# Kernel optimization log

Hardware: AMD Instinct MI355X
Metric: run time of the kernel (lower is better)

## Reference

```python
import jax, jax.numpy as jnp
import numpy as np

B, D, N = 2, 256, 8192   # batch, in_channels, sequence length
CI = 128                 # inter_channels
BN_EPS = 1e-5


def conv1x1(w, b, x):
    # w: (Cout, Cin), b: (Cout,), x: (B, Cin, N) -> (B, Cout, N)
    return jnp.einsum('oc,bcn->bon', w, x) + b[None, :, None]


def maxpool2(x):
    # MaxPool1d(kernel_size=2): (B, C, N) -> (B, C, N//2)
    b, c, n = x.shape
    return x.reshape(b, c, n // 2, 2).max(axis=-1)


def setup_inputs() -> dict:
    key = jax.random.key(0)
    ks = jax.random.split(key, 11)
    s_in = 1.0 / np.sqrt(D)
    s_ci = 1.0 / np.sqrt(CI)
    return {
        'f': jax.random.normal(ks[0], (B, D, N), dtype=jnp.float32),
        'g_w': jax.random.uniform(ks[1], (CI, D), jnp.float32, -s_in, s_in),
        'g_b': jax.random.uniform(ks[2], (CI,), jnp.float32, -s_in, s_in),
        'theta_w': jax.random.uniform(ks[3], (CI, D), jnp.float32, -s_in, s_in),
        'theta_b': jax.random.uniform(ks[4], (CI,), jnp.float32, -s_in, s_in),
        'phi_w': jax.random.uniform(ks[5], (CI, D), jnp.float32, -s_in, s_in),
        'phi_b': jax.random.uniform(ks[6], (CI,), jnp.float32, -s_in, s_in),
        'W_w': jax.random.uniform(ks[7], (D, CI), jnp.float32, -s_ci, s_ci),
        'W_b': jax.random.uniform(ks[8], (D,), jnp.float32, -s_ci, s_ci),
        'bn_gamma': jax.random.normal(ks[9], (D,), dtype=jnp.float32) * 0.1,
        'bn_beta': jax.random.normal(ks[10], (D,), dtype=jnp.float32) * 0.1,
    }


def reference(f, g_w, g_b, theta_w, theta_b, phi_w, phi_b, W_w, W_b, bn_gamma, bn_beta):
    # projections (1x1 convs); g and phi are sub-sampled by maxpool(2)
    g_f = maxpool2(conv1x1(g_w, g_b, f))          # (B, CI, N/2)
    theta_f = conv1x1(theta_w, theta_b, f)        # (B, CI, N)
    phi_f = maxpool2(conv1x1(phi_w, phi_b, f))    # (B, CI, N/2)

    # affinity: theta^T @ phi, softmax over keys (no scale, as in source)
    A = jnp.einsum('bcn,bcm->bnm', theta_f, phi_f)     # (B, N, N/2)
    A = jax.nn.softmax(A, axis=-1)
    y = jnp.einsum('bnm,bcm->bcn', A, g_f)             # (B, CI, N)

    # W: 1x1 conv + BatchNorm1d (training-mode batch stats), residual
    Wy = conv1x1(W_w, W_b, y)                          # (B, D, N)
    mean = Wy.mean(axis=(0, 2), keepdims=True)
    var = Wy.var(axis=(0, 2), keepdims=True)           # biased, like torch BN
    Wy = (Wy - mean) * jax.lax.rsqrt(var + BN_EPS)
    Wy = Wy * bn_gamma[None, :, None] + bn_beta[None, :, None]
    return Wy + f
```

## Files before the change

### kernel.cpp

```cpp
#include <hip/hip_runtime.h>
#include <hip/hip_bf16.h>
#include <math.h>

#define B_ 2
#define D_ 256
#define N_ 8192
#define CI_ 128
#define M_ 4096
#define BN_EPS_ 1e-5f
#define LOG2E_ 1.4426950408889634f

#define GLOBAL_AS __attribute__((address_space(1)))
#define LDS_AS __attribute__((address_space(3)))

#define OFF_WALL 0
#define OFF_THT  65536
#define OFF_PHT  (OFF_THT + 1048576)
#define OFF_GT   (OFF_PHT + 524288)
#define OFF_YP   (OFF_GT  + 524288)

typedef __attribute__((ext_vector_type(8))) short bfrag;
typedef __attribute__((ext_vector_type(4))) float f4v;
typedef __attribute__((ext_vector_type(16))) float f16v;
typedef __attribute__((ext_vector_type(4))) short s4v;
typedef __attribute__((ext_vector_type(4))) unsigned u4v;

__device__ inline unsigned short bf16rne(float x) {
    unsigned u = __float_as_uint(x);
    u += 0x7fff + ((u >> 16) & 1);
    return (unsigned short)(u >> 16);
}

__device__ inline float exp2fast(float x) {
    float r;
    asm("v_exp_f32 %0, %1" : "=v"(r) : "v"(x));
    return r;
}

__global__ __launch_bounds__(256) void wconv_kernel(
    const float* __restrict__ gw, const float* __restrict__ tw, const float* __restrict__ pw,
    const float* __restrict__ Ww, short* __restrict__ wall)
{
    int idx = blockIdx.x * 256 + threadIdx.x;
    int which = idx >> 15;
    int rem = idx & 32767;
    const float* src = (which == 0) ? gw : (which == 1) ? tw : (which == 2) ? pw : Ww;
    float v = src[rem];
    if (which == 1) v *= LOG2E_;
    wall[idx] = (short)bf16rne(v);
}

__global__ __launch_bounds__(256, 2) void proj_kernel(
    const float* __restrict__ f, const short* __restrict__ wall,
    const float* __restrict__ tb, const float* __restrict__ gb, const float* __restrict__ pb,
    short* __restrict__ th_t, short* __restrict__ g_t, short* __restrict__ ph_t)
{
    __shared__ short sF[32 * 72];

    const int tid = threadIdx.x;
    const int wave = tid >> 6, lane = tid & 63;
    const int lq = lane & 15, quad = lane >> 4;
    const int b = blockIdx.y;
    const int n0 = blockIdx.x * 32;

    const float* fb = f + (size_t)b * D_ * N_;

    f4v acc[6][2];
#pragma unroll
    for (int ct = 0; ct < 6; ct++)
#pragma unroll
        for (int nf = 0; nf < 2; nf++) acc[ct][nf] = (f4v){0.f, 0.f, 0.f, 0.f};

    const int sn = tid & 31;
    const int sgrp = tid >> 5;

    for (int kc = 0; kc < D_; kc += 64) {
        __syncthreads();
#pragma unroll
        for (int jj = 0; jj < 4; jj++) {
            int dd = kc + sgrp * 8 + 2 * jj;
            float v0 = fb[(size_t)dd * N_ + n0 + sn];
            float v1 = fb[(size_t)(dd + 1) * N_ + n0 + sn];
            unsigned pk = (unsigned)bf16rne(v0) | ((unsigned)bf16rne(v1) << 16);
            *(unsigned*)&sF[sn * 72 + sgrp * 8 + 2 * jj] = pk;
        }
        __syncthreads();

        bfrag afr[6][2], bfr[2][2];
#pragma unroll
        for (int ks = 0; ks < 2; ks++) {
#pragma unroll
            for (int nf = 0; nf < 2; nf++)
                bfr[nf][ks] = *(const bfrag*)&sF[(nf * 16 + lq) * 72 + ks * 32 + quad * 8];
#pragma unroll
            for (int ct = 0; ct < 6; ct++)
                afr[ct][ks] = *(const bfrag*)&wall[(wave * 96 + ct * 16 + lq) * 256 + kc + ks * 32 + quad * 8];
        }
#pragma unroll
        for (int ks = 0; ks < 2; ks++)
#pragma unroll
            for (int ct = 0; ct < 6; ct++) {
                acc[ct][0] = __builtin_amdgcn_mfma_f32_16x16x32_bf16(afr[ct][ks], bfr[0][ks], acc[ct][0], 0, 0, 0);
                acc[ct][1] = __builtin_amdgcn_mfma_f32_16x16x32_bf16(afr[ct][ks], bfr[1][ks], acc[ct][1], 0, 0, 0);
            }
    }

#pragma unroll
    for (int ct = 0; ct < 6; ct++) {
        const int cf = wave * 6 + ct;
#pragma unroll
        for (int nf = 0; nf < 2; nf++) {
            f4v v = acc[ct][nf];
            const int n = n0 + nf * 16 + lq;
            if (cf < 8) {
                const int cb = cf * 16 + quad * 4;
                float pl[4];
#pragma unroll
                for (int r = 0; r < 4; r++) {
                    float o = __shfl_xor(v[r], 1);
                    pl[r] = fmaxf(v[r], o) + gb[cb + r];
                }
                if (!(lq & 1)) {
                    const int m = n >> 1;
#pragma unroll
                    for (int r = 0; r < 4; r++)
                        g_t[((size_t)b * CI_ + cb + r) * M_ + m] = (short)bf16rne(pl[r]);
                }
            } else if (cf < 16) {
                const int cb = (cf - 8) * 16 + quad * 4;
                s4v o;
#pragma unroll
                for (int r = 0; r < 4; r++) o[r] = (short)bf16rne(v[r] + tb[cb + r] * LOG2E_);
                *(s4v*)&th_t[((size_t)b * N_ + n) * CI_ + cb] = o;
            } else {
                const int cb = (cf - 16) * 16 + quad * 4;
                float pl[4];
#pragma unroll
                for (int r = 0; r < 4; r++) {
                    float o = __shfl_xor(v[r], 1);
                    pl[r] = fmaxf(v[r], o) + pb[cb + r];
                }
                if (!(lq & 1)) {
                    const int m = n >> 1;
                    s4v o;
#pragma unroll
                    for (int r = 0; r < 4; r++) o[r] = (short)bf16rne(pl[r]);
                    *(s4v*)&ph_t[((size_t)b * M_ + m) * CI_ + cb] = o;
                }
            }
        }
    }
}

template<int NS>
__global__ __launch_bounds__(256, 3) void attn_kernel(
    const short* __restrict__ th_p, const short* __restrict__ ph_p,
    const short* __restrict__ g_p, short* __restrict__ yp, float* __restrict__ ml)
{
    constexpr int SK = M_ / NS;
    __shared__ short sPh[64 * 128];
    __shared__ short sG [2][128 * 72];

    const int tid = threadIdx.x;
    const int wave = tid >> 6, lane = tid & 63;
    const int l = lane & 31, h = lane >> 5;

    const int bid = blockIdx.x;
    const int pair = bid & (2 * NS - 1);
    const int b = pair & 1;
    const int split = pair >> 1;
    const int q0 = (bid / (2 * NS)) * 128;
    const int qg = q0 + wave * 32 + l;

    const short* thr = th_p + ((size_t)b * N_ + qg) * CI_;
    bfrag tf[8];
#pragma unroll
    for (int s = 0; s < 8; s++)
        tf[s] = *(const bfrag*)&thr[s * 16 + h * 8];

    f16v yacc[4];
#pragma unroll
    for (int ct = 0; ct < 4; ct++)
#pragma unroll
        for (int r = 0; r < 16; r++) yacc[ct][r] = 0.f;
    float mI = -INFINITY, lI = 0.f;

    const short* phg = ph_p + (size_t)b * M_ * CI_;
    const short* gg  = g_p + (size_t)b * CI_ * M_;

    const int k0 = split * SK;
    const int xm = l & 15;

    const int prow = (lane >> 4);
    const int pslot = lane & 15;

    const int i0 = (wave < 2) ? wave * 5 : 10 + (wave - 2) * 4;
    const int nIss = (wave < 2) ? 5 : 4;
    int gsrc[5];
#pragma unroll
    for (int p = 0; p < 5; p++) {
        const int t = (i0 + p) * 64 + lane;
        gsrc[p] = (t / 9) * M_ + (t % 9) * 8;
    }

#define STAGE_PHI(KC)                                                                       \
    do {                                                                                    \
        _Pragma("unroll")                                                                   \
        for (int p = 0; p < 4; p++) {                                                       \
            const int rp = wave * 16 + p * 4 + prow;                     \
            const int cg = pslot ^ (p * 4 + prow);                   \
            __builtin_amdgcn_global_load_lds(                                               \
                (const GLOBAL_AS void*)(phg + (size_t)((KC) + rp) * 128 + cg * 8),          \
                (LDS_AS void*)(&sPh[(wave * 16 + p * 4) * 128]), 16, 0, 0);                 \
        }                                                                                   \
    } while (0)
#define STAGE_G(BUF, KC)                                                                    \
    do {                                                                                    \
        _Pragma("unroll")                                                                   \
        for (int p = 0; p < 5; p++) {                                                       \
            if (p < nIss)                                                                   \
                __builtin_amdgcn_global_load_lds(                                           \
                    (const GLOBAL_AS void*)(gg + gsrc[p] + (KC)),                           \
                    (LDS_AS void*)(&sG[BUF][(i0 + p) * 512]), 16, 0, 0);                    \
        }                                                                                   \
    } while (0)

    STAGE_PHI(k0);
    STAGE_G(0, k0);

    int cur = 0;
    for (int kc = k0; kc < k0 + SK; kc += 64) {
        __syncthreads();
        const bool nxt = (kc + 64 < k0 + SK);
        if (nxt) {
            STAGE_G(cur ^ 1, kc + 64);
            __builtin_amdgcn_sched_barrier(0);
        }

        f16v sv[2];
        __builtin_amdgcn_s_setprio(1);
#pragma unroll
        for (int kt = 0; kt < 2; kt++) {
            f16v a;
#pragma unroll
            for (int r = 0; r < 16; r++) a[r] = 0.f;
#pragma unroll
            for (int s = 0; s < 8; s++) {
                bfrag pa = *(const bfrag*)&sPh[(kt * 32 + l) * 128 + (((s << 1) | h) ^ xm) * 8];
                a = __builtin_amdgcn_mfma_f32_32x32x16_bf16(pa, tf[s], a, 0, 0, 0);
            }
            sv[kt] = a;
        }
        __builtin_amdgcn_s_setprio(0);

        __builtin_amdgcn_sched_barrier(0);
        __builtin_amdgcn_s_barrier();
        if (nxt) {
            STAGE_PHI(kc + 64);
            __builtin_amdgcn_sched_barrier(0);
        }

        float mx;
        {
            float t[16];
#pragma unroll
            for (int r = 0; r < 16; r++) t[r] = fmaxf(sv[0][r], sv[1][r]);
#pragma unroll
            for (int st = 8; st > 0; st >>= 1)
#pragma unroll
                for (int r = 0; r < st; r++) t[r] = fmaxf(t[r], t[r + st]);
            mx = fmaxf(t[0], __shfl_xor(t[0], 32));
        }

        if (__any(mx > mI + 8.f)) {
            float mnew = fmaxf(mI, mx);
            float al = exp2fast(mI - mnew);
            lI *= al;
#pragma unroll
            for (int ct = 0; ct < 4; ct++)
#pragma unroll
                for (int r = 0; r < 16; r++) yacc[ct][r] *= al;
            mI = mnew;
        }

        float ps = 0.f;
        bfrag pf[4];
#pragma unroll
        for (int s = 0; s < 4; s++) {
            const int kt = s >> 1;
            const int rb = (s & 1) * 8;
            float p[8];
#pragma unroll
            for (int j = 0; j < 8; j++) p[j] = exp2fast(sv[kt][rb + j] - mI);
            ps += ((p[0] + p[1]) + (p[2] + p[3])) + ((p[4] + p[5]) + (p[6] + p[7]));
            unsigned w0, w1, w2, w3;
            asm("v_cvt_pk_bf16_f32 %0, %1, %2" : "=v"(w0) : "v"(p[0]), "v"(p[1]));
            asm("v_cvt_pk_bf16_f32 %0, %1, %2" : "=v"(w1) : "v"(p[2]), "v"(p[3]));
            asm("v_cvt_pk_bf16_f32 %0, %1, %2" : "=v"(w2) : "v"(p[4]), "v"(p[5]));
            asm("v_cvt_pk_bf16_f32 %0, %1, %2" : "=v"(w3) : "v"(p[6]), "v"(p[7]));
            unsigned O0 = h ? w2 : w0;
            unsigned O1 = h ? w3 : w1;
            unsigned Xs0 = h ? w0 : w2;
            unsigned Xs1 = h ? w1 : w3;
            unsigned X0 = (unsigned)__shfl_xor((int)Xs0, 32);
            unsigned X1 = (unsigned)__shfl_xor((int)Xs1, 32);
            u4v t;
            t.x = h ? X0 : O0;
            t.y = h ? X1 : O1;
            t.z = h ? O0 : X0;
            t.w = h ? O1 : X1;
            pf[s] = __builtin_bit_cast(bfrag, t);
        }
        ps += __shfl_xor(ps, 32);
        lI += ps;

        __builtin_amdgcn_s_setprio(1);
#pragma unroll
        for (int ct = 0; ct < 4; ct++)
#pragma unroll
            for (int s = 0; s < 4; s++) {
                bfrag ga = *(const bfrag*)&sG[cur][(ct * 32 + l) * 72 + s * 16 + h * 8];
                yacc[ct] = __builtin_amdgcn_mfma_f32_32x32x16_bf16(ga, pf[s], yacc[ct], 0, 0, 0);
            }
        __builtin_amdgcn_s_setprio(0);

        cur ^= 1;
    }
#undef STAGE_PHI
#undef STAGE_G

    short* yb = yp + (((size_t)split * B_ + b) * N_) * CI_;
#pragma unroll
    for (int ct = 0; ct < 4; ct++)
#pragma unroll
        for (int rq = 0; rq < 4; rq++) {
            const int c0 = ct * 32 + 8 * rq + 4 * h;
            s4v o;
#pragma unroll
            for (int j = 0; j < 4; j++) o[j] = (short)bf16rne(yacc[ct][rq * 4 + j]);
            *(s4v*)&yb[(size_t)qg * CI_ + c0] = o;
        }
    if (h == 0) {
        float* mlb = ml + ((split * B_ + b) * 2) * N_;
        mlb[qg] = mI;
        mlb[N_ + qg] = lI;
    }
}

template<int NS>
__global__ __launch_bounds__(256) void wy_merge_kernel(
    const short* __restrict__ yp, const float* __restrict__ ml,
    const short* __restrict__ wall2, const float* __restrict__ Wb,
    float* __restrict__ out)
{
    const int tid = threadIdx.x;
    const int wave = tid >> 6, lane = tid & 63;
    const int l = lane & 31, h = lane >> 5;
    const int b = blockIdx.y;
    const int n = blockIdx.x * 32 + l;

    float m[NS], lv[NS];
#pragma unroll
    for (int sp = 0; sp < NS; sp++) {
        const float* mlb = ml + ((sp * B_ + b) * 2) * N_;
        m[sp] = mlb[n];
        lv[sp] = mlb[N_ + n];
    }
    float mmax = m[0];
#pragma unroll
    for (int sp = 1; sp < NS; sp++) mmax = fmaxf(mmax, m[sp]);
    float e[NS], den = 0.f;
#pragma unroll
    for (int sp = 0; sp < NS; sp++) { e[sp] = exp2fast(m[sp] - mmax); den += lv[sp] * e[sp]; }
    float inv = 1.0f / den;
#pragma unroll
    for (int sp = 0; sp < NS; sp++) e[sp] *= inv;

    bfrag by[8];
#pragma unroll
    for (int s = 0; s < 8; s++) {
        float a[8];
#pragma unroll
        for (int j = 0; j < 8; j++) a[j] = 0.f;
#pragma unroll
        for (int sp = 0; sp < NS; sp++) {
            bfrag yv = *(const bfrag*)&yp[(((size_t)sp * B_ + b) * N_ + n) * CI_ + s * 16 + h * 8];
            u4v u = __builtin_bit_cast(u4v, yv);
#pragma unroll
            for (int p = 0; p < 4; p++) {
                a[2 * p]     = fmaf(e[sp], __uint_as_float(u[p] << 16), a[2 * p]);
                a[2 * p + 1] = fmaf(e[sp], __uint_as_float(u[p] & 0xffff0000u), a[2 * p + 1]);
            }
        }
        u4v pk;
#pragma unroll
        for (int p = 0; p < 4; p++) {
            unsigned r;
            asm("v_cvt_pk_bf16_f32 %0, %1, %2" : "=v"(r) : "v"(a[2 * p]), "v"(a[2 * p + 1]));
            pk[p] = r;
        }
        by[s] = __builtin_bit_cast(bfrag, pk);
    }

    f16v acc[2];
#pragma unroll
    for (int rt = 0; rt < 2; rt++)
#pragma unroll
        for (int r = 0; r < 16; r++) acc[rt][r] = 0.f;

#pragma unroll
    for (int s = 0; s < 8; s++)
#pragma unroll
        for (int rt = 0; rt < 2; rt++) {
            bfrag aw = *(const bfrag*)&wall2[((wave * 2 + rt) * 32 + l) * 128 + s * 16 + h * 8];
            acc[rt] = __builtin_amdgcn_mfma_f32_32x32x16_bf16(aw, by[s], acc[rt], 0, 0, 0);
        }

#pragma unroll
    for (int rt = 0; rt < 2; rt++)
#pragma unroll
        for (int r = 0; r < 16; r++) {
            const int d = (wave * 2 + rt) * 32 + (r & 3) + 8 * (r >> 2) + 4 * h;
            out[((size_t)b * D_ + d) * N_ + n] = acc[rt][r] + Wb[d];
        }
}

__global__ __launch_bounds__(256) void stats_kernel(
    const float* __restrict__ wy, float* __restrict__ mean, float* __restrict__ rstd)
{
    __shared__ float ssum[256], ssq[256];
    int d = blockIdx.x;
    int tid = threadIdx.x;
    float s = 0.f, sq = 0.f;
    for (int b = 0; b < B_; b++) {
        const float4* p = (const float4*)(wy + (size_t)b * D_ * N_ + (size_t)d * N_);
        for (int i = tid; i < N_ / 4; i += 256) {
            float4 v = p[i];
            s += v.x + v.y + v.z + v.w;
            sq = fmaf(v.x, v.x, sq);
            sq = fmaf(v.y, v.y, sq);
            sq = fmaf(v.z, v.z, sq);
            sq = fmaf(v.w, v.w, sq);
        }
    }
    ssum[tid] = s; ssq[tid] = sq;
    __syncthreads();
    for (int st = 128; st > 0; st >>= 1) {
        if (tid < st) { ssum[tid] += ssum[tid + st]; ssq[tid] += ssq[tid + st]; }
        __syncthreads();
    }
    if (tid == 0) {
        float inv = 1.0f / (float)(B_ * N_);
        float mn = ssum[0] * inv;
        float var = ssq[0] * inv - mn * mn;
        mean[d] = mn;
        rstd[d] = rsqrtf(var + BN_EPS_);
    }
}

__global__ __launch_bounds__(256) void bn_res_kernel(
    float* __restrict__ out, const float* __restrict__ f,
    const float* __restrict__ mean, const float* __restrict__ rstd,
    const float* __restrict__ gamma, const float* __restrict__ beta)
{
    int i = blockIdx.x * 256 + threadIdx.x;
    size_t e = (size_t)i * 4;
    int d = (int)((e >> 13) & 255);
    float4 wy = ((const float4*)out)[i];
    float4 ff = ((const float4*)f)[i];
    float sc = rstd[d] * gamma[d];
    float mn = mean[d];
    float bt = beta[d];
    float4 r;
    r.x = (wy.x - mn) * sc + bt + ff.x;
    r.y = (wy.y - mn) * sc + bt + ff.y;
    r.z = (wy.z - mn) * sc + bt + ff.z;
    r.w = (wy.w - mn) * sc + bt + ff.w;
    ((float4*)out)[i] = r;
}

extern "C" void kernel_launch(void* const* d_in, const int* in_sizes, int n_in,
                              void* d_out, int out_size, void* d_ws, size_t ws_size,
                              hipStream_t stream)
{
    const float* f   = (const float*)d_in[0];
    const float* g_w = (const float*)d_in[1];
    const float* g_b = (const float*)d_in[2];
    const float* t_w = (const float*)d_in[3];
    const float* t_b = (const float*)d_in[4];
    const float* p_w = (const float*)d_in[5];
    const float* p_b = (const float*)d_in[6];
    const float* W_w = (const float*)d_in[7];
    const float* W_b = (const float*)d_in[8];
    const float* gam = (const float*)d_in[9];
    const float* bet = (const float*)d_in[10];
    float* out = (float*)d_out;
    float* ws = (float*)d_ws;

    const size_t need8 = ((size_t)OFF_YP + 8u * 1048576u + 8u * 32768u + 512u) * 4u;
    const int ns = (ws_size >= need8) ? 8 : 4;

    short* wall  = (short*)(ws + OFF_WALL);
    short* wall2 = wall + 3 * 32768;
    short* th_t = (short*)(ws + OFF_THT);
    short* ph_t = (short*)(ws + OFF_PHT);
    short* g_t  = (short*)(ws + OFF_GT);
    short* ypart = (short*)(ws + OFF_YP);
    float* mlp = ws + OFF_YP + (size_t)ns * 1048576u;
    float* mnp = mlp + (size_t)ns * 32768u;
    float* rsp = mnp + 256;

    wconv_kernel<<<512, 256, 0, stream>>>(g_w, t_w, p_w, W_w, wall);
    proj_kernel<<<dim3(N_ / 32, B_), 256, 0, stream>>>(f, wall, t_b, g_b, p_b,
                                                       th_t, g_t, ph_t);
    if (ns == 8) {
        attn_kernel<8><<<1024, 256, 0, stream>>>(th_t, ph_t, g_t, ypart, mlp);
        wy_merge_kernel<8><<<dim3(N_ / 32, B_), 256, 0, stream>>>(ypart, mlp, wall2, W_b, out);
    } else {
        attn_kernel<4><<<512, 256, 0, stream>>>(th_t, ph_t, g_t, ypart, mlp);
        wy_merge_kernel<4><<<dim3(N_ / 32, B_), 256, 0, stream>>>(ypart, mlp, wall2, W_b, out);
    }
    stats_kernel<<<D_, 256, 0, stream>>>(out, mnp, rsp);
    bn_res_kernel<<<(B_ * D_ * N_ / 4) / 256, 256, 0, stream>>>(out, f, mnp, rsp, gam, bet);
}
```

Measured before the change: 208.2 us.

## Double-buffer phi and g tiles with 32-key chunks and six-way key split

The attention kernel now processes keys in 32-wide chunks and double-buffers both the phi and g tiles in LDS, issued together in one DMA stage, which removes the mid-iteration barrier that was needed before re-staging phi. The key split changes from 8 to 6 (768 blocks, uneven 704/672 chunk sizes) to better match CU count and to reduce partial-result merge traffic. Smaller chunks mean more loop iterations and barriers per key, and less MFMA work between softmax rescale checks.

```diff
diff --git a/kernel.cpp b/kernel.cpp
--- a/kernel.cpp
+++ b/kernel.cpp
@@ -157,21 +157,28 @@
     const short* __restrict__ th_p, const short* __restrict__ ph_p,
     const short* __restrict__ g_p, short* __restrict__ yp, float* __restrict__ ml)
 {
-    constexpr int SK = M_ / NS;
-    __shared__ short sPh[64 * 128];
-    __shared__ short sG [2][128 * 72];
+    __shared__ short sPh[2][32 * 128];
+    __shared__ short sG [2][128 * 40];
 
     const int tid = threadIdx.x;
     const int wave = tid >> 6, lane = tid & 63;
     const int l = lane & 31, h = lane >> 5;
 
     const int bid = blockIdx.x;
-    const int pair = bid & (2 * NS - 1);
+    const int pair = bid % (2 * NS);
     const int b = pair & 1;
     const int split = pair >> 1;
     const int q0 = (bid / (2 * NS)) * 128;
     const int qg = q0 + wave * 32 + l;
 
+    int k0, SK;
+    if (NS == 6) {
+        if (split < 2) { SK = 704; k0 = split * 704; }
+        else           { SK = 672; k0 = 1408 + (split - 2) * 672; }
+    } else {
+        SK = M_ / NS; k0 = split * SK;
+    }
+
     const short* thr = th_p + ((size_t)b * N_ + qg) * CI_;
     bfrag tf[8];
 #pragma unroll
@@ -188,36 +195,32 @@
     const short* phg = ph_p + (size_t)b * M_ * CI_;
     const short* gg  = g_p + (size_t)b * CI_ * M_;
 
-    const int k0 = split * SK;
     const int xm = l & 15;
 
     const int prow = (lane >> 4);
     const int pslot = lane & 15;
 
-    const int i0 = (wave < 2) ? wave * 5 : 10 + (wave - 2) * 4;
-    const int nIss = (wave < 2) ? 5 : 4;
-    int gsrc[5];
-#pragma unroll
-    for (int p = 0; p < 5; p++) {
+    const int i0 = (wave < 2) ? wave * 3 : 6 + (wave - 2) * 2;
+    const int nIss = (wave < 2) ? 3 : 2;
+    int gsrc[3];
+#pragma unroll
+    for (int p = 0; p < 3; p++) {
         const int t = (i0 + p) * 64 + lane;
-        gsrc[p] = (t / 9) * M_ + (t % 9) * 8;
-    }
-
-#define STAGE_PHI(KC)                                                                       \
+        gsrc[p] = (t / 5) * M_ + (t % 5) * 8;
+    }
+
+#define STAGE_DMA(BUF, KC)                                                                  \
     do {                                                                                    \
         _Pragma("unroll")                                                                   \
-        for (int p = 0; p < 4; p++) {                                                       \
-            const int rp = wave * 16 + p * 4 + prow;                     \
-            const int cg = pslot ^ (p * 4 + prow);                   \
+        for (int p = 0; p < 2; p++) {                                                       \
+            const int rp = wave * 8 + p * 4 + prow;                      \
+            const int cg = pslot ^ (rp & 15);                        \
             __builtin_amdgcn_global_load_lds(                                               \
                 (const GLOBAL_AS void*)(phg + (size_t)((KC) + rp) * 128 + cg * 8),          \
-                (LDS_AS void*)(&sPh[(wave * 16 + p * 4) * 128]), 16, 0, 0);                 \
+                (LDS_AS void*)(&sPh[BUF][(wave * 8 + p * 4) * 128]), 16, 0, 0);             \
         }                                                                                   \
-    } while (0)
-#define STAGE_G(BUF, KC)                                                                    \
-    do {                                                                                    \
         _Pragma("unroll")                                                                   \
-        for (int p = 0; p < 5; p++) {                                                       \
+        for (int p = 0; p < 3; p++) {                                                       \
             if (p < nIss)                                                                   \
                 __builtin_amdgcn_global_load_lds(                                           \
                     (const GLOBAL_AS void*)(gg + gsrc[p] + (KC)),                           \
@@ -225,48 +228,35 @@
         }                                                                                   \
     } while (0)
 
-    STAGE_PHI(k0);
-    STAGE_G(0, k0);
+    STAGE_DMA(0, k0);
 
     int cur = 0;
-    for (int kc = k0; kc < k0 + SK; kc += 64) {
+    for (int kc = k0; kc < k0 + SK; kc += 32) {
         __syncthreads();
-        const bool nxt = (kc + 64 < k0 + SK);
+        const bool nxt = (kc + 32 < k0 + SK);
         if (nxt) {
-            STAGE_G(cur ^ 1, kc + 64);
+            STAGE_DMA(cur ^ 1, kc + 32);
             __builtin_amdgcn_sched_barrier(0);
         }
 
-        f16v sv[2];
+        f16v sv;
+#pragma unroll
+        for (int r = 0; r < 16; r++) sv[r] = 0.f;
         __builtin_amdgcn_s_setprio(1);
 #pragma unroll
-        for (int kt = 0; kt < 2; kt++) {
-            f16v a;
-#pragma unroll
-            for (int r = 0; r < 16; r++) a[r] = 0.f;
-#pragma unroll
-            for (int s = 0; s < 8; s++) {
-                bfrag pa = *(const bfrag*)&sPh[(kt * 32 + l) * 128 + (((s << 1) | h) ^ xm) * 8];
-                a = __builtin_amdgcn_mfma_f32_32x32x16_bf16(pa, tf[s], a, 0, 0, 0);
-            }
-            sv[kt] = a;
+        for (int s = 0; s < 8; s++) {
+            bfrag pa = *(const bfrag*)&sPh[cur][l * 128 + (((s << 1) | h) ^ xm) * 8];
+            sv = __builtin_amdgcn_mfma_f32_32x32x16_bf16(pa, tf[s], sv, 0, 0, 0);
         }
         __builtin_amdgcn_s_setprio(0);
-
-        __builtin_amdgcn_sched_barrier(0);
-        __builtin_amdgcn_s_barrier();
-        if (nxt) {
-            STAGE_PHI(kc + 64);
-            __builtin_amdgcn_sched_barrier(0);
-        }
 
         float mx;
         {
-            float t[16];
-#pragma unroll
-            for (int r = 0; r < 16; r++) t[r] = fmaxf(sv[0][r], sv[1][r]);
-#pragma unroll
-            for (int st = 8; st > 0; st >>= 1)
+            float t[8];
+#pragma unroll
+            for (int r = 0; r < 8; r++) t[r] = fmaxf(sv[r], sv[r + 8]);
+#pragma unroll
+            for (int st = 4; st > 0; st >>= 1)
 #pragma unroll
                 for (int r = 0; r < st; r++) t[r] = fmaxf(t[r], t[r + st]);
             mx = fmaxf(t[0], __shfl_xor(t[0], 32));
@@ -284,14 +274,13 @@
         }
 
         float ps = 0.f;
-        bfrag pf[4];
-#pragma unroll
-        for (int s = 0; s < 4; s++) {
-            const int kt = s >> 1;
-            const int rb = (s & 1) * 8;
+        bfrag pf[2];
+#pragma unroll
+        for (int s = 0; s < 2; s++) {
+            const int rb = s * 8;
             float p[8];
 #pragma unroll
-            for (int j = 0; j < 8; j++) p[j] = exp2fast(sv[kt][rb + j] - mI);
+            for (int j = 0; j < 8; j++) p[j] = exp2fast(sv[rb + j] - mI);
             ps += ((p[0] + p[1]) + (p[2] + p[3])) + ((p[4] + p[5]) + (p[6] + p[7]));
             unsigned w0, w1, w2, w3;
             asm("v_cvt_pk_bf16_f32 %0, %1, %2" : "=v"(w0) : "v"(p[0]), "v"(p[1]));
@@ -318,16 +307,15 @@
 #pragma unroll
         for (int ct = 0; ct < 4; ct++)
 #pragma unroll
-            for (int s = 0; s < 4; s++) {
-                bfrag ga = *(const bfrag*)&sG[cur][(ct * 32 + l) * 72 + s * 16 + h * 8];
+            for (int s = 0; s < 2; s++) {
+                bfrag ga = *(const bfrag*)&sG[cur][(ct * 32 + l) * 40 + s * 16 + h * 8];
                 yacc[ct] = __builtin_amdgcn_mfma_f32_32x32x16_bf16(ga, pf[s], yacc[ct], 0, 0, 0);
             }
         __builtin_amdgcn_s_setprio(0);
 
         cur ^= 1;
     }
-#undef STAGE_PHI
-#undef STAGE_G
+#undef STAGE_DMA
 
     short* yb = yp + (((size_t)split * B_ + b) * N_) * CI_;
 #pragma unroll
@@ -497,8 +485,8 @@
     float* out = (float*)d_out;
     float* ws = (float*)d_ws;
 
-    const size_t need8 = ((size_t)OFF_YP + 8u * 1048576u + 8u * 32768u + 512u) * 4u;
-    const int ns = (ws_size >= need8) ? 8 : 4;
+    const size_t need6 = ((size_t)OFF_YP + 6u * 1048576u + 6u * 32768u + 512u) * 4u;
+    const int ns = (ws_size >= need6) ? 6 : 4;
 
     short* wall  = (short*)(ws + OFF_WALL);
     short* wall2 = wall + 3 * 32768;
@@ -513,9 +501,9 @@
     wconv_kernel<<<512, 256, 0, stream>>>(g_w, t_w, p_w, W_w, wall);
     proj_kernel<<<dim3(N_ / 32, B_), 256, 0, stream>>>(f, wall, t_b, g_b, p_b,
                                                        th_t, g_t, ph_t);
-    if (ns == 8) {
-        attn_kernel<8><<<1024, 256, 0, stream>>>(th_t, ph_t, g_t, ypart, mlp);
-        wy_merge_kernel<8><<<dim3(N_ / 32, B_), 256, 0, stream>>>(ypart, mlp, wall2, W_b, out);
+    if (ns == 6) {
+        attn_kernel<6><<<768, 256, 0, stream>>>(th_t, ph_t, g_t, ypart, mlp);
+        wy_merge_kernel<6><<<dim3(N_ / 32, B_), 256, 0, stream>>>(ypart, mlp, wall2, W_b, out);
     } else {
         attn_kernel<4><<<512, 256, 0, stream>>>(th_t, ph_t, g_t, ypart, mlp);
         wy_merge_kernel<4><<<dim3(N_ / 32, B_), 256, 0, stream>>>(ypart, mlp, wall2, W_b, out);
```

Measured after the change: 185.6 us. 1.12x faster.
